# Optimization experiments

Hardware: AMD Instinct MI355X
Metric: run time of the kernel (lower is better)

Reference implementation:

```python
import jax, jax.numpy as jnp
import numpy as np

N = 20000   # nodes
E = 320000  # edges
F = 64      # input node features
H = 256     # hidden_layer_size
C = 10      # nbr_classes
G = 64      # graphs in the batch


def _lin(key, fan_in, fan_out):
    k1, k2 = jax.random.split(key)
    bound = 1.0 / np.sqrt(fan_in)
    W = jax.random.uniform(k1, (fan_in, fan_out), jnp.float32, -bound, bound)
    b = jax.random.uniform(k2, (fan_out,), jnp.float32, -bound, bound)
    return W, b


def setup_inputs() -> dict:
    key = jax.random.key(0)
    ks = jax.random.split(key, 10)
    x = jax.random.normal(ks[0], (N, F), jnp.float32)
    edge_index = jax.random.randint(ks[1], (2, E), 0, N)
    batch = jnp.sort(jax.random.randint(ks[2], (N,), 0, G))
    W1, b1 = _lin(ks[3], F, H)
    W2, b2 = _lin(ks[4], H, H)
    W3, b3 = _lin(ks[5], H, H)
    W4, b4 = _lin(ks[6], H, H)
    W5, b5 = _lin(ks[7], H, H)
    Wout, bout = _lin(ks[8], H, C)
    return {"x": x, "edge_index": edge_index, "batch": batch,
            "W1": W1, "b1": b1, "W2": W2, "b2": b2, "W3": W3, "b3": b3,
            "W4": W4, "b4": b4, "W5": W5, "b5": b5, "Wout": Wout, "bout": bout}


def reference(x, edge_index, batch, W1, b1, W2, b2, W3, b3, W4, b4, W5, b5, Wout, bout):
    # GCNConv (Kipf & Welling): add self-loops, D^{-1/2}(A+I)D^{-1/2} (X W) + b.
    # Dropout(p=0.5) is identity in eval mode (reference is deterministic).
    loop = jnp.arange(N)
    row = jnp.concatenate([edge_index[0], loop])  # source nodes, [E+N]
    col = jnp.concatenate([edge_index[1], loop])  # target nodes, [E+N]
    deg = jax.ops.segment_sum(jnp.ones(E + N, x.dtype), col, num_segments=N)
    dinv = jax.lax.rsqrt(deg)  # deg >= 1 thanks to self-loops
    norm = (dinv[row] * dinv[col])[:, None]  # [E+N, 1]

    def gcn_conv(h, W, b):
        m = (h @ W)[row] * norm                      # gather + normalize, [E+N, H]
        return jax.ops.segment_sum(m, col, num_segments=N) + b

    h = x
    for W, b in ((W1, b1), (W2, b2), (W3, b3), (W4, b4), (W5, b5)):
        h = jax.nn.relu(gcn_conv(h, W, b))

    # global_mean_pool over graph ids
    counts = jax.ops.segment_sum(jnp.ones(N, h.dtype), batch, num_segments=G)
    pooled = jax.ops.segment_sum(h, batch, num_segments=G) / jnp.maximum(counts, 1.0)[:, None]
    return pooled @ Wout + bout  # [G, C]
```

## Files before the change

### kernel.cpp

```cpp
#include <hip/hip_runtime.h>

#define NN 20000
#define NE 320000
#define FIN 64
#define HD 256
#define NC 10
#define NG 64
#define NB ((NN + 255) / 256)
#define EBMAX (NE + 15 * NN + 16)

typedef unsigned short u16;
typedef unsigned int u32;
typedef __attribute__((ext_vector_type(8))) short short8;
typedef __attribute__((ext_vector_type(4))) float f32x4;

__device__ __forceinline__ float bf2f(u16 u) {
    union { u32 i; float f; } v; v.i = ((u32)u) << 16; return v.f;
}
__device__ __forceinline__ u16 f2bf(float f) {
    union { float f; u32 i; } v; v.f = f;
    u32 r = v.i + 0x7fffu + ((v.i >> 16) & 1u);
    return (u16)(r >> 16);
}

__global__ void k_degpad(const int* __restrict__ col, int* __restrict__ degi,
                         const int* __restrict__ batch, int* __restrict__ gstart,
                         u32* __restrict__ ebuf32) {
    int i = blockIdx.x * 256 + threadIdx.x;
    if (i < NE) atomicAdd(&degi[col[i]], 1);
    if (i < NN) {
        int b = batch[i];
        int prev = (i == 0) ? -1 : batch[i - 1];
        if (b != prev) gstart[b] = i;
    }
    if (i < EBMAX / 2) ebuf32[i] = 0x4E204E20u;
}

__global__ __launch_bounds__(256) void k_scan1(const int* __restrict__ degi,
                                               int* __restrict__ rowptr,
                                               int* __restrict__ bsum) {
    int t = threadIdx.x;
    int i = blockIdx.x * 256 + t;
    int v = (i < NN) ? ((degi[i] + 15) & ~15) : 0;
    int lane = t & 63, wid = t >> 6;
    int x = v;
#pragma unroll
    for (int off = 1; off < 64; off <<= 1) {
        int y = __shfl_up(x, off);
        if (lane >= off) x += y;
    }
    __shared__ int ws[4];
    if (lane == 63) ws[wid] = x;
    __syncthreads();
    int woff = 0;
    for (int w = 0; w < wid; ++w) woff += ws[w];
    if (i < NN) rowptr[i] = woff + x - v;
    if (t == 255) bsum[blockIdx.x] = woff + x;
}

__global__ void k_scan3(const int* __restrict__ degi, const int* __restrict__ bsum,
                        int* __restrict__ rowptr, int* __restrict__ cursor,
                        float* __restrict__ dinv,
                        const float* __restrict__ x, u16* __restrict__ u0) {
    __shared__ int pref[NB];
    if (threadIdx.x < NB) pref[threadIdx.x] = bsum[threadIdx.x];
    __syncthreads();
    if (threadIdx.x == 0) {
        int run = 0;
        for (int k = 0; k < NB; ++k) { int t = pref[k]; pref[k] = run; run += t; }
    }
    __syncthreads();
    int i = blockIdx.x * 256 + threadIdx.x;
    if (i < NN) {
        int dg = degi[i];
        int rp = rowptr[i] + pref[i >> 8];
        rowptr[i] = rp;
        cursor[i] = rp;
        dinv[i] = rsqrtf((float)(1 + dg));
        if (i == NN - 1) rowptr[NN] = rp + ((dg + 15) & ~15);
    }
    if (i < NN * FIN / 4) {
        int node = i >> 4;
        float d = rsqrtf((float)(1 + degi[node]));
        float4 v = *(const float4*)&x[(size_t)i * 4];
        u32 lo = (u32)f2bf(v.x * d) | ((u32)f2bf(v.y * d) << 16);
        u32 hi = (u32)f2bf(v.z * d) | ((u32)f2bf(v.w * d) << 16);
        *(uint2*)&u0[(size_t)i * 4] = make_uint2(lo, hi);
    }
    if (blockIdx.x == 0 && threadIdx.x < FIN) u0[(size_t)NN * FIN + threadIdx.x] = 0;
}

__global__ void k_fill(const int* __restrict__ row, const int* __restrict__ col,
                       int* __restrict__ cursor, u16* __restrict__ ebuf) {
    int e = blockIdx.x * 256 + threadIdx.x;
    if (e < NE) {
        int c = col[e];
        int pos = atomicAdd(&cursor[c], 1);
        ebuf[pos] = (u16)row[e];
    }
}

__global__ __launch_bounds__(256) void k_trans(const float* __restrict__ W0, const float* __restrict__ W1,
                                               const float* __restrict__ W2, const float* __restrict__ W3,
                                               const float* __restrict__ W4,
                                               u16* __restrict__ T0, u16* __restrict__ T1,
                                               u16* __restrict__ T2, u16* __restrict__ T3,
                                               u16* __restrict__ T4) {
    int l = blockIdx.z;
    const float* W = (l == 0) ? W0 : (l == 1) ? W1 : (l == 2) ? W2 : (l == 3) ? W3 : W4;
    u16* T = (l == 0) ? T0 : (l == 1) ? T1 : (l == 2) ? T2 : (l == 3) ? T3 : T4;
    int K = (l == 0) ? FIN : HD;
    int k0 = blockIdx.x * 32;
    if (k0 >= K) return;
    int n0 = blockIdx.y * 32;
    __shared__ float tile[32][33];
    int tx = threadIdx.x & 31, ty = threadIdx.x >> 5;
#pragma unroll
    for (int r = 0; r < 32; r += 8)
        tile[ty + r][tx] = W[(size_t)(k0 + ty + r) * HD + n0 + tx];
    __syncthreads();
#pragma unroll
    for (int r = 0; r < 32; r += 8)
        T[(size_t)(n0 + ty + r) * K + k0 + tx] = f2bf(tile[tx][ty + r]);
}

__global__ __launch_bounds__(512, 8) void k_fused(const u16* __restrict__ U,
                                                  const int* __restrict__ rowptr,
                                                  const u16* __restrict__ ebuf,
                                                  const float* __restrict__ dinv,
                                                  const u16* __restrict__ Wt,
                                                  const float* __restrict__ bias,
                                                  u16* __restrict__ O,
                                                  int K, int scaleOut) {
    __shared__ u16 Asm[16][264];
    __shared__ float bs[HD];
    const int m0 = blockIdx.x * 16;
    const int t = threadIdx.x;
    const int wave = t >> 6;
    const int lane = t & 63;
    if (t < HD) bs[t] = bias[t];
    if (blockIdx.x == 0 && t < HD) O[(size_t)NN * HD + t] = 0;

    if (K == HD) {
        const int grp = lane >> 4;
        const int seg = lane & 15;
        for (int tk = 0; tk < 4; ++tk) {
            const int task = wave + tk * 8;
            const int row = task & 15;
            const int n = m0 + row;
            const int fbase = (task >> 4) * 128 + seg * 8;
            const int s = rowptr[n], e = rowptr[n + 1];
            float acc[8];
            if (grp == 0) {
                uint4 v = *(const uint4*)&U[(size_t)n * HD + fbase];
                acc[0] = bf2f((u16)(v.x & 0xffff)); acc[1] = bf2f((u16)(v.x >> 16));
                acc[2] = bf2f((u16)(v.y & 0xffff)); acc[3] = bf2f((u16)(v.y >> 16));
                acc[4] = bf2f((u16)(v.z & 0xffff)); acc[5] = bf2f((u16)(v.z >> 16));
                acc[6] = bf2f((u16)(v.w & 0xffff)); acc[7] = bf2f((u16)(v.w >> 16));
            } else {
#pragma unroll
                for (int k = 0; k < 8; ++k) acc[k] = 0.f;
            }
            for (int j = s; j < e; j += 16) {
                uint2 idv = *(const uint2*)&ebuf[j + grp * 4];
                int r0 = (int)(idv.x & 0xffff), r1 = (int)(idv.x >> 16);
                int r2 = (int)(idv.y & 0xffff), r3 = (int)(idv.y >> 16);
                uint4 v[4];
                v[0] = *(const uint4*)&U[(size_t)r0 * HD + fbase];
                v[1] = *(const uint4*)&U[(size_t)r1 * HD + fbase];
                v[2] = *(const uint4*)&U[(size_t)r2 * HD + fbase];
                v[3] = *(const uint4*)&U[(size_t)r3 * HD + fbase];
#pragma unroll
                for (int k = 0; k < 4; ++k) {
                    acc[0] += bf2f((u16)(v[k].x & 0xffff)); acc[1] += bf2f((u16)(v[k].x >> 16));
                    acc[2] += bf2f((u16)(v[k].y & 0xffff)); acc[3] += bf2f((u16)(v[k].y >> 16));
                    acc[4] += bf2f((u16)(v[k].z & 0xffff)); acc[5] += bf2f((u16)(v[k].z >> 16));
                    acc[6] += bf2f((u16)(v[k].w & 0xffff)); acc[7] += bf2f((u16)(v[k].w >> 16));
                }
            }
#pragma unroll
            for (int k = 0; k < 8; ++k) {
                acc[k] += __shfl_xor(acc[k], 16);
                acc[k] += __shfl_xor(acc[k], 32);
            }
            if (grp == 0) {
                float d = dinv[n];
                uint4 o;
                o.x = (u32)f2bf(acc[0] * d) | ((u32)f2bf(acc[1] * d) << 16);
                o.y = (u32)f2bf(acc[2] * d) | ((u32)f2bf(acc[3] * d) << 16);
                o.z = (u32)f2bf(acc[4] * d) | ((u32)f2bf(acc[5] * d) << 16);
                o.w = (u32)f2bf(acc[6] * d) | ((u32)f2bf(acc[7] * d) << 16);
                *(uint4*)&Asm[row][fbase] = o;
            }
        }
    } else {
        const int grp = lane >> 3;
        const int seg = lane & 7;
        for (int task = wave; task < 16; task += 8) {
            const int n = m0 + task;
            const int s = rowptr[n], e = rowptr[n + 1];
            float acc[8];
            if (grp == 0) {
                uint4 v = *(const uint4*)&U[(size_t)n * FIN + seg * 8];
                acc[0] = bf2f((u16)(v.x & 0xffff)); acc[1] = bf2f((u16)(v.x >> 16));
                acc[2] = bf2f((u16)(v.y & 0xffff)); acc[3] = bf2f((u16)(v.y >> 16));
                acc[4] = bf2f((u16)(v.z & 0xffff)); acc[5] = bf2f((u16)(v.z >> 16));
                acc[6] = bf2f((u16)(v.w & 0xffff)); acc[7] = bf2f((u16)(v.w >> 16));
            } else {
#pragma unroll
                for (int k = 0; k < 8; ++k) acc[k] = 0.f;
            }
            for (int j = s; j < e; j += 16) {
                int r0 = (int)ebuf[j + grp];
                int r1 = (int)ebuf[j + 8 + grp];
                uint4 v0 = *(const uint4*)&U[(size_t)r0 * FIN + seg * 8];
                uint4 v1 = *(const uint4*)&U[(size_t)r1 * FIN + seg * 8];
                acc[0] += bf2f((u16)(v0.x & 0xffff)); acc[1] += bf2f((u16)(v0.x >> 16));
                acc[2] += bf2f((u16)(v0.y & 0xffff)); acc[3] += bf2f((u16)(v0.y >> 16));
                acc[4] += bf2f((u16)(v0.z & 0xffff)); acc[5] += bf2f((u16)(v0.z >> 16));
                acc[6] += bf2f((u16)(v0.w & 0xffff)); acc[7] += bf2f((u16)(v0.w >> 16));
                acc[0] += bf2f((u16)(v1.x & 0xffff)); acc[1] += bf2f((u16)(v1.x >> 16));
                acc[2] += bf2f((u16)(v1.y & 0xffff)); acc[3] += bf2f((u16)(v1.y >> 16));
                acc[4] += bf2f((u16)(v1.z & 0xffff)); acc[5] += bf2f((u16)(v1.z >> 16));
                acc[6] += bf2f((u16)(v1.w & 0xffff)); acc[7] += bf2f((u16)(v1.w >> 16));
            }
#pragma unroll
            for (int off = 8; off < 64; off <<= 1)
#pragma unroll
                for (int k = 0; k < 8; ++k) acc[k] += __shfl_xor(acc[k], off);
            if (grp == 0) {
                float d = dinv[n];
                uint4 o;
                o.x = (u32)f2bf(acc[0] * d) | ((u32)f2bf(acc[1] * d) << 16);
                o.y = (u32)f2bf(acc[2] * d) | ((u32)f2bf(acc[3] * d) << 16);
                o.z = (u32)f2bf(acc[4] * d) | ((u32)f2bf(acc[5] * d) << 16);
                o.w = (u32)f2bf(acc[6] * d) | ((u32)f2bf(acc[7] * d) << 16);
                *(uint4*)&Asm[task][seg * 8] = o;
            }
        }
    }
    __syncthreads();

    const int quad = lane >> 4;
    const int l16 = lane & 15;
    const int n0 = wave * 32;
    f32x4 acc[2];
#pragma unroll
    for (int j = 0; j < 2; ++j) acc[j] = (f32x4){0.f, 0.f, 0.f, 0.f};

#pragma unroll 2
    for (int k0 = 0; k0 < K; k0 += 32) {
        short8 a = *(const short8*)&Asm[l16][k0 + quad * 8];
        short8 b0 = *(const short8*)&Wt[(size_t)(n0 + l16) * K + k0 + quad * 8];
        short8 b1 = *(const short8*)&Wt[(size_t)(n0 + 16 + l16) * K + k0 + quad * 8];
        acc[0] = __builtin_amdgcn_mfma_f32_16x16x32_bf16(a, b0, acc[0], 0, 0, 0);
        acc[1] = __builtin_amdgcn_mfma_f32_16x16x32_bf16(a, b1, acc[1], 0, 0, 0);
    }
#pragma unroll
    for (int r = 0; r < 4; ++r) {
        int m = m0 + quad * 4 + r;
        float d = scaleOut ? dinv[m] : 1.0f;
#pragma unroll
        for (int j = 0; j < 2; ++j) {
            int n = n0 + j * 16 + l16;
            float val = fmaxf(acc[j][r] + bs[n], 0.f) * d;
            O[(size_t)m * HD + n] = f2bf(val);
        }
    }
}

__global__ __launch_bounds__(512) void k_poolout(const u16* __restrict__ h,
                                                 const int* __restrict__ gstart,
                                                 const float* __restrict__ Wout,
                                                 const float* __restrict__ bout,
                                                 float* __restrict__ out) {
    int g = blockIdx.x;
    int t = threadIdx.x;
    int f = t & (HD - 1);
    int half = t >> 8;
    __shared__ float pp[2][HD];
    __shared__ float pooled[HD];
    __shared__ float part[NC][16];
    __shared__ int s_se[2];
    if (t == 0) {
        int st = gstart[g];
        int en = NN;
        for (int gg = g + 1; gg < NG; ++gg) en = min(en, gstart[gg]);
        s_se[0] = st; s_se[1] = en;
    }
    __syncthreads();
    int st = s_se[0], en = s_se[1];
    float a0 = 0.f, a1 = 0.f, a2 = 0.f, a3 = 0.f;
    int n = st + half;
    for (; n + 6 < en; n += 8) {
        a0 += bf2f(h[(size_t)n * HD + f]);
        a1 += bf2f(h[(size_t)(n + 2) * HD + f]);
        a2 += bf2f(h[(size_t)(n + 4) * HD + f]);
        a3 += bf2f(h[(size_t)(n + 6) * HD + f]);
    }
    for (; n < en; n += 2) a0 += bf2f(h[(size_t)n * HD + f]);
    pp[half][f] = a0 + a1 + a2 + a3;
    __syncthreads();
    if (t < HD) {
        float inv = 1.0f / (float)max(en - st, 1);
        pooled[t] = (pp[0][t] + pp[1][t]) * inv;
    }
    __syncthreads();
    if (t < NC * 16) {
        int c = t >> 4, l16 = t & 15;
        float s = 0.f;
        for (int ff = l16; ff < HD; ff += 16)
            s = fmaf(pooled[ff], Wout[(size_t)ff * NC + c], s);
        part[c][l16] = s;
    }
    __syncthreads();
    if (t < NC) {
        float s = 0.f;
#pragma unroll
        for (int k = 0; k < 16; ++k) s += part[t][k];
        out[(size_t)g * NC + t] = s + bout[t];
    }
}

extern "C" void kernel_launch(void* const* d_in, const int* in_sizes, int n_in,
                              void* d_out, int out_size, void* d_ws, size_t ws_size,
                              hipStream_t stream) {
    const float* x     = (const float*)d_in[0];
    const int*   ei    = (const int*)d_in[1];
    const int*   batch = (const int*)d_in[2];
    const float* Wl[5] = {(const float*)d_in[3], (const float*)d_in[5], (const float*)d_in[7],
                          (const float*)d_in[9], (const float*)d_in[11]};
    const float* bl[5] = {(const float*)d_in[4], (const float*)d_in[6], (const float*)d_in[8],
                          (const float*)d_in[10], (const float*)d_in[12]};
    const float* Wout = (const float*)d_in[13];
    const float* bout = (const float*)d_in[14];
    float* out = (float*)d_out;

    const int* row = ei;
    const int* col = ei + NE;

    char* p = (char*)d_ws;
    auto take = [&](size_t bytes) { char* q = p; p += (bytes + 255) & ~(size_t)255; return q; };
    float* dinv   = (float*)take(NN * 4);
    int*   degi   = (int*)take(NN * 4);
    int*   rowptr = (int*)take((NN + 1) * 4);
    int*   cursor = (int*)take(NN * 4);
    int*   bsum   = (int*)take(NB * 4);
    u16*   ebuf   = (u16*)take(EBMAX * 2);
    int*   gstart = (int*)take(NG * 4);
    u16*   Wt[5];
    for (int l = 0; l < 5; ++l) Wt[l] = (u16*)take((size_t)HD * HD * 2);
    u16*   B1     = (u16*)take((size_t)(NN + 1) * HD * 2);
    u16*   B2     = (u16*)take((size_t)(NN + 1) * HD * 2);

    hipMemsetAsync(degi, 0, NN * 4, stream);
    hipMemsetAsync(gstart, 0x7F, NG * 4, stream);
    k_degpad<<<(NE + 255) / 256, 256, 0, stream>>>(col, degi, batch, gstart, (u32*)ebuf);
    k_scan1<<<NB, 256, 0, stream>>>(degi, rowptr, bsum);
    k_scan3<<<(NN * FIN / 4 + 255) / 256, 256, 0, stream>>>(degi, bsum, rowptr, cursor, dinv, x, B1);
    k_fill<<<(NE + 255) / 256, 256, 0, stream>>>(row, col, cursor, ebuf);
    dim3 tGrid(8, 8, 5);
    k_trans<<<tGrid, 256, 0, stream>>>(Wl[0], Wl[1], Wl[2], Wl[3], Wl[4],
                                       Wt[0], Wt[1], Wt[2], Wt[3], Wt[4]);

    const int fGrid = NN / 16;
    k_fused<<<fGrid, 512, 0, stream>>>(B1, rowptr, ebuf, dinv, Wt[0], bl[0], B2, FIN, 1);
    k_fused<<<fGrid, 512, 0, stream>>>(B2, rowptr, ebuf, dinv, Wt[1], bl[1], B1, HD, 1);
    k_fused<<<fGrid, 512, 0, stream>>>(B1, rowptr, ebuf, dinv, Wt[2], bl[2], B2, HD, 1);
    k_fused<<<fGrid, 512, 0, stream>>>(B2, rowptr, ebuf, dinv, Wt[3], bl[3], B1, HD, 1);
    k_fused<<<fGrid, 512, 0, stream>>>(B1, rowptr, ebuf, dinv, Wt[4], bl[4], B2, HD, 0);

    k_poolout<<<NG, 512, 0, stream>>>(B2, gstart, Wout, bout, out);
}
```

Baseline: 367.6 us.

## Software-pipeline neighbor gathers across tasks and stage weights through LDS

The 256-wide aggregation now reads all row pointers and the first edge-index batch up front, then prefetches the next task's first neighbor rows and self row while the current task accumulates. Inside each task the next edge-index chunk is loaded before the current rows are summed. The MFMA loop now copies each 32-wide K slice of the transposed weights into a new shared buffer with two barriers per step, instead of each wave reading weights straight from global memory. Occupancy hint drops from 8 to 6 to fit the extra registers and LDS, which may reduce latency hiding, and the per-slice barriers add sync cost.

```diff
diff --git a/kernel.cpp b/kernel.cpp
--- a/kernel.cpp
+++ b/kernel.cpp
@@ -21,6 +21,21 @@
     union { float f; u32 i; } v; v.f = f;
     u32 r = v.i + 0x7fffu + ((v.i >> 16) & 1u);
     return (u16)(r >> 16);
+}
+
+__device__ __forceinline__ void accum8(float* acc, const uint4& v) {
+    acc[0] += bf2f((u16)(v.x & 0xffff)); acc[1] += bf2f((u16)(v.x >> 16));
+    acc[2] += bf2f((u16)(v.y & 0xffff)); acc[3] += bf2f((u16)(v.y >> 16));
+    acc[4] += bf2f((u16)(v.z & 0xffff)); acc[5] += bf2f((u16)(v.z >> 16));
+    acc[6] += bf2f((u16)(v.w & 0xffff)); acc[7] += bf2f((u16)(v.w >> 16));
+}
+__device__ __forceinline__ void loadrows(uint4* v, uint2 id, const u16* __restrict__ U, int fb) {
+    int r0 = (int)(id.x & 0xffff), r1 = (int)(id.x >> 16);
+    int r2 = (int)(id.y & 0xffff), r3 = (int)(id.y >> 16);
+    v[0] = *(const uint4*)&U[(size_t)r0 * HD + fb];
+    v[1] = *(const uint4*)&U[(size_t)r1 * HD + fb];
+    v[2] = *(const uint4*)&U[(size_t)r2 * HD + fb];
+    v[3] = *(const uint4*)&U[(size_t)r3 * HD + fb];
 }
 
 __global__ void k_degpad(const int* __restrict__ col, int* __restrict__ degi,
@@ -124,7 +139,7 @@
         T[(size_t)(n0 + ty + r) * K + k0 + tx] = f2bf(tile[tx][ty + r]);
 }
 
-__global__ __launch_bounds__(512, 8) void k_fused(const u16* __restrict__ U,
+__global__ __launch_bounds__(512, 6) void k_fused(const u16* __restrict__ U,
                                                   const int* __restrict__ rowptr,
                                                   const u16* __restrict__ ebuf,
                                                   const float* __restrict__ dinv,
@@ -133,6 +148,7 @@
                                                   u16* __restrict__ O,
                                                   int K, int scaleOut) {
     __shared__ u16 Asm[16][264];
+    __shared__ u16 Bsm[256][40];
     __shared__ float bs[HD];
     const int m0 = blockIdx.x * 16;
     const int t = threadIdx.x;
@@ -144,39 +160,58 @@
     if (K == HD) {
         const int grp = lane >> 4;
         const int seg = lane & 15;
+        int n_[4], s_[4], e_[4], fb_[4];
+#pragma unroll
         for (int tk = 0; tk < 4; ++tk) {
             const int task = wave + tk * 8;
-            const int row = task & 15;
-            const int n = m0 + row;
-            const int fbase = (task >> 4) * 128 + seg * 8;
-            const int s = rowptr[n], e = rowptr[n + 1];
+            n_[tk] = m0 + (task & 15);
+            fb_[tk] = (task >> 4) * 128 + seg * 8;
+        }
+#pragma unroll
+        for (int tk = 0; tk < 4; ++tk) {
+            s_[tk] = rowptr[n_[tk]];
+            e_[tk] = rowptr[n_[tk] + 1];
+        }
+        uint2 id_[4];
+#pragma unroll
+        for (int tk = 0; tk < 4; ++tk)
+            id_[tk] = (s_[tk] < e_[tk]) ? *(const uint2*)&ebuf[s_[tk] + grp * 4]
+                                        : make_uint2(0x4E204E20u, 0x4E204E20u);
+        uint4 va[4], sla;
+        loadrows(va, id_[0], U, fb_[0]);
+        sla = *(const uint4*)&U[(size_t)n_[0] * HD + fb_[0]];
+#pragma unroll
+        for (int tk = 0; tk < 4; ++tk) {
+            uint4 vb[4], slb;
+            if (tk < 3) {
+                loadrows(vb, id_[tk + 1], U, fb_[tk + 1]);
+                slb = *(const uint4*)&U[(size_t)n_[tk + 1] * HD + fb_[tk + 1]];
+            } else {
+                vb[0] = vb[1] = vb[2] = vb[3] = make_uint4(0u, 0u, 0u, 0u);
+                slb = make_uint4(0u, 0u, 0u, 0u);
+            }
             float acc[8];
             if (grp == 0) {
-                uint4 v = *(const uint4*)&U[(size_t)n * HD + fbase];
-                acc[0] = bf2f((u16)(v.x & 0xffff)); acc[1] = bf2f((u16)(v.x >> 16));
-                acc[2] = bf2f((u16)(v.y & 0xffff)); acc[3] = bf2f((u16)(v.y >> 16));
-                acc[4] = bf2f((u16)(v.z & 0xffff)); acc[5] = bf2f((u16)(v.z >> 16));
-                acc[6] = bf2f((u16)(v.w & 0xffff)); acc[7] = bf2f((u16)(v.w >> 16));
+                acc[0] = bf2f((u16)(sla.x & 0xffff)); acc[1] = bf2f((u16)(sla.x >> 16));
+                acc[2] = bf2f((u16)(sla.y & 0xffff)); acc[3] = bf2f((u16)(sla.y >> 16));
+                acc[4] = bf2f((u16)(sla.z & 0xffff)); acc[5] = bf2f((u16)(sla.z >> 16));
+                acc[6] = bf2f((u16)(sla.w & 0xffff)); acc[7] = bf2f((u16)(sla.w >> 16));
             } else {
 #pragma unroll
                 for (int k = 0; k < 8; ++k) acc[k] = 0.f;
             }
-            for (int j = s; j < e; j += 16) {
-                uint2 idv = *(const uint2*)&ebuf[j + grp * 4];
-                int r0 = (int)(idv.x & 0xffff), r1 = (int)(idv.x >> 16);
-                int r2 = (int)(idv.y & 0xffff), r3 = (int)(idv.y >> 16);
-                uint4 v[4];
-                v[0] = *(const uint4*)&U[(size_t)r0 * HD + fbase];
-                v[1] = *(const uint4*)&U[(size_t)r1 * HD + fbase];
-                v[2] = *(const uint4*)&U[(size_t)r2 * HD + fbase];
-                v[3] = *(const uint4*)&U[(size_t)r3 * HD + fbase];
-#pragma unroll
-                for (int k = 0; k < 4; ++k) {
-                    acc[0] += bf2f((u16)(v[k].x & 0xffff)); acc[1] += bf2f((u16)(v[k].x >> 16));
-                    acc[2] += bf2f((u16)(v[k].y & 0xffff)); acc[3] += bf2f((u16)(v[k].y >> 16));
-                    acc[4] += bf2f((u16)(v[k].z & 0xffff)); acc[5] += bf2f((u16)(v[k].z >> 16));
-                    acc[6] += bf2f((u16)(v[k].w & 0xffff)); acc[7] += bf2f((u16)(v[k].w >> 16));
-                }
+            int j = s_[tk] + 16;
+            bool more = j < e_[tk];
+            uint2 idn = make_uint2(0x4E204E20u, 0x4E204E20u);
+            if (more) idn = *(const uint2*)&ebuf[j + grp * 4];
+            accum8(acc, va[0]); accum8(acc, va[1]); accum8(acc, va[2]); accum8(acc, va[3]);
+            while (more) {
+                uint4 vx[4];
+                loadrows(vx, idn, U, fb_[tk]);
+                j += 16;
+                more = j < e_[tk];
+                if (more) idn = *(const uint2*)&ebuf[j + grp * 4];
+                accum8(acc, vx[0]); accum8(acc, vx[1]); accum8(acc, vx[2]); accum8(acc, vx[3]);
             }
 #pragma unroll
             for (int k = 0; k < 8; ++k) {
@@ -184,14 +219,17 @@
                 acc[k] += __shfl_xor(acc[k], 32);
             }
             if (grp == 0) {
-                float d = dinv[n];
+                float d = dinv[n_[tk]];
                 uint4 o;
                 o.x = (u32)f2bf(acc[0] * d) | ((u32)f2bf(acc[1] * d) << 16);
                 o.y = (u32)f2bf(acc[2] * d) | ((u32)f2bf(acc[3] * d) << 16);
                 o.z = (u32)f2bf(acc[4] * d) | ((u32)f2bf(acc[5] * d) << 16);
                 o.w = (u32)f2bf(acc[6] * d) | ((u32)f2bf(acc[7] * d) << 16);
-                *(uint4*)&Asm[row][fbase] = o;
-            }
+                *(uint4*)&Asm[n_[tk] - m0][fb_[tk]] = o;
+            }
+#pragma unroll
+            for (int k = 0; k < 4; ++k) va[k] = vb[k];
+            sla = slb;
         }
     } else {
         const int grp = lane >> 3;
@@ -215,14 +253,8 @@
                 int r1 = (int)ebuf[j + 8 + grp];
                 uint4 v0 = *(const uint4*)&U[(size_t)r0 * FIN + seg * 8];
                 uint4 v1 = *(const uint4*)&U[(size_t)r1 * FIN + seg * 8];
-                acc[0] += bf2f((u16)(v0.x & 0xffff)); acc[1] += bf2f((u16)(v0.x >> 16));
-                acc[2] += bf2f((u16)(v0.y & 0xffff)); acc[3] += bf2f((u16)(v0.y >> 16));
-                acc[4] += bf2f((u16)(v0.z & 0xffff)); acc[5] += bf2f((u16)(v0.z >> 16));
-                acc[6] += bf2f((u16)(v0.w & 0xffff)); acc[7] += bf2f((u16)(v0.w >> 16));
-                acc[0] += bf2f((u16)(v1.x & 0xffff)); acc[1] += bf2f((u16)(v1.x >> 16));
-                acc[2] += bf2f((u16)(v1.y & 0xffff)); acc[3] += bf2f((u16)(v1.y >> 16));
-                acc[4] += bf2f((u16)(v1.z & 0xffff)); acc[5] += bf2f((u16)(v1.z >> 16));
-                acc[6] += bf2f((u16)(v1.w & 0xffff)); acc[7] += bf2f((u16)(v1.w >> 16));
+                accum8(acc, v0);
+                accum8(acc, v1);
             }
 #pragma unroll
             for (int off = 8; off < 64; off <<= 1)
@@ -248,13 +280,24 @@
 #pragma unroll
     for (int j = 0; j < 2; ++j) acc[j] = (f32x4){0.f, 0.f, 0.f, 0.f};
 
-#pragma unroll 2
     for (int k0 = 0; k0 < K; k0 += 32) {
+        {
+            int r = t >> 1, h16 = (t & 1) * 16;
+#pragma unroll
+            for (int j = 0; j < 2; ++j) {
+                float4 v = *(const float4*)&Wt[(size_t)r * K + k0 + h16 + j * 8];
+                *(float4*)&Bsm[r][h16 + j * 8] = v;
+            }
+        }
+        __syncthreads();
         short8 a = *(const short8*)&Asm[l16][k0 + quad * 8];
-        short8 b0 = *(const short8*)&Wt[(size_t)(n0 + l16) * K + k0 + quad * 8];
-        short8 b1 = *(const short8*)&Wt[(size_t)(n0 + 16 + l16) * K + k0 + quad * 8];
-        acc[0] = __builtin_amdgcn_mfma_f32_16x16x32_bf16(a, b0, acc[0], 0, 0, 0);
-        acc[1] = __builtin_amdgcn_mfma_f32_16x16x32_bf16(a, b1, acc[1], 0, 0, 0);
+        short8 b[2];
+#pragma unroll
+        for (int j = 0; j < 2; ++j) b[j] = *(const short8*)&Bsm[n0 + j * 16 + l16][quad * 8];
+#pragma unroll
+        for (int j = 0; j < 2; ++j)
+            acc[j] = __builtin_amdgcn_mfma_f32_16x16x32_bf16(a, b[j], acc[j], 0, 0, 0);
+        __syncthreads();
     }
 #pragma unroll
     for (int r = 0; r < 4; ++r) {
```

Result: slower. 414.5 us (+12.8%).

## Pad edge lists to 8, shuffle-broadcast neighbor ids, stage weights in LDS

Applied to the files above, without the earlier changes.

Each node's edge list is now padded to a multiple of 8 instead of 16. This cuts the wasted gathers of the zero sentinel row in both aggregation paths. In the 256-wide path, the first 8 lanes load neighbor ids once and broadcast them with shuffles, and the row/half task mapping is reordered. The MFMA loop now stages each 32-wide K-slice of the transposed weights through a new shared-memory buffer with barriers, instead of each wave reading its slice straight from global memory. The extra LDS and barriers may lower occupancy and add sync overhead, since there is little reuse of that slice across waves.

```diff
diff --git a/kernel.cpp b/kernel.cpp
--- a/kernel.cpp
+++ b/kernel.cpp
@@ -7,7 +7,7 @@
 #define NC 10
 #define NG 64
 #define NB ((NN + 255) / 256)
-#define EBMAX (NE + 15 * NN + 16)
+#define EBMAX (NE + 7 * NN + 8)
 
 typedef unsigned short u16;
 typedef unsigned int u32;
@@ -21,6 +21,12 @@
     union { float f; u32 i; } v; v.f = f;
     u32 r = v.i + 0x7fffu + ((v.i >> 16) & 1u);
     return (u16)(r >> 16);
+}
+__device__ __forceinline__ void accum8(float* acc, const uint4& v) {
+    acc[0] += bf2f((u16)(v.x & 0xffff)); acc[1] += bf2f((u16)(v.x >> 16));
+    acc[2] += bf2f((u16)(v.y & 0xffff)); acc[3] += bf2f((u16)(v.y >> 16));
+    acc[4] += bf2f((u16)(v.z & 0xffff)); acc[5] += bf2f((u16)(v.z >> 16));
+    acc[6] += bf2f((u16)(v.w & 0xffff)); acc[7] += bf2f((u16)(v.w >> 16));
 }
 
 __global__ void k_degpad(const int* __restrict__ col, int* __restrict__ degi,
@@ -41,7 +47,7 @@
                                                int* __restrict__ bsum) {
     int t = threadIdx.x;
     int i = blockIdx.x * 256 + t;
-    int v = (i < NN) ? ((degi[i] + 15) & ~15) : 0;
+    int v = (i < NN) ? ((degi[i] + 7) & ~7) : 0;
     int lane = t & 63, wid = t >> 6;
     int x = v;
 #pragma unroll
@@ -77,7 +83,7 @@
         rowptr[i] = rp;
         cursor[i] = rp;
         dinv[i] = rsqrtf((float)(1 + dg));
-        if (i == NN - 1) rowptr[NN] = rp + ((dg + 15) & ~15);
+        if (i == NN - 1) rowptr[NN] = rp + ((dg + 7) & ~7);
     }
     if (i < NN * FIN / 4) {
         int node = i >> 4;
@@ -133,6 +139,7 @@
                                                   u16* __restrict__ O,
                                                   int K, int scaleOut) {
     __shared__ u16 Asm[16][264];
+    __shared__ u16 Bsm[256][40];
     __shared__ float bs[HD];
     const int m0 = blockIdx.x * 16;
     const int t = threadIdx.x;
@@ -144,11 +151,10 @@
     if (K == HD) {
         const int grp = lane >> 4;
         const int seg = lane & 15;
-        for (int tk = 0; tk < 4; ++tk) {
-            const int task = wave + tk * 8;
-            const int row = task & 15;
+        for (int task = wave; task < 32; task += 8) {
+            const int row = task >> 1;
             const int n = m0 + row;
-            const int fbase = (task >> 4) * 128 + seg * 8;
+            const int fbase = (task & 1) * 128 + seg * 8;
             const int s = rowptr[n], e = rowptr[n + 1];
             float acc[8];
             if (grp == 0) {
@@ -161,22 +167,16 @@
 #pragma unroll
                 for (int k = 0; k < 8; ++k) acc[k] = 0.f;
             }
-            for (int j = s; j < e; j += 16) {
-                uint2 idv = *(const uint2*)&ebuf[j + grp * 4];
-                int r0 = (int)(idv.x & 0xffff), r1 = (int)(idv.x >> 16);
-                int r2 = (int)(idv.y & 0xffff), r3 = (int)(idv.y >> 16);
-                uint4 v[4];
-                v[0] = *(const uint4*)&U[(size_t)r0 * HD + fbase];
-                v[1] = *(const uint4*)&U[(size_t)r1 * HD + fbase];
-                v[2] = *(const uint4*)&U[(size_t)r2 * HD + fbase];
-                v[3] = *(const uint4*)&U[(size_t)r3 * HD + fbase];
-#pragma unroll
-                for (int k = 0; k < 4; ++k) {
-                    acc[0] += bf2f((u16)(v[k].x & 0xffff)); acc[1] += bf2f((u16)(v[k].x >> 16));
-                    acc[2] += bf2f((u16)(v[k].y & 0xffff)); acc[3] += bf2f((u16)(v[k].y >> 16));
-                    acc[4] += bf2f((u16)(v[k].z & 0xffff)); acc[5] += bf2f((u16)(v[k].z >> 16));
-                    acc[6] += bf2f((u16)(v[k].w & 0xffff)); acc[7] += bf2f((u16)(v[k].w >> 16));
+            for (int j = s; j < e; j += 8) {
+                int myid = (lane < 8) ? (int)ebuf[j + lane] : 0;
+                uint4 v[2];
+#pragma unroll
+                for (int k = 0; k < 2; ++k) {
+                    int r = __shfl(myid, grp * 2 + k);
+                    v[k] = *(const uint4*)&U[(size_t)r * HD + fbase];
                 }
+                accum8(acc, v[0]);
+                accum8(acc, v[1]);
             }
 #pragma unroll
             for (int k = 0; k < 8; ++k) {
@@ -210,19 +210,10 @@
 #pragma unroll
                 for (int k = 0; k < 8; ++k) acc[k] = 0.f;
             }
-            for (int j = s; j < e; j += 16) {
+            for (int j = s; j < e; j += 8) {
                 int r0 = (int)ebuf[j + grp];
-                int r1 = (int)ebuf[j + 8 + grp];
                 uint4 v0 = *(const uint4*)&U[(size_t)r0 * FIN + seg * 8];
-                uint4 v1 = *(const uint4*)&U[(size_t)r1 * FIN + seg * 8];
-                acc[0] += bf2f((u16)(v0.x & 0xffff)); acc[1] += bf2f((u16)(v0.x >> 16));
-                acc[2] += bf2f((u16)(v0.y & 0xffff)); acc[3] += bf2f((u16)(v0.y >> 16));
-                acc[4] += bf2f((u16)(v0.z & 0xffff)); acc[5] += bf2f((u16)(v0.z >> 16));
-                acc[6] += bf2f((u16)(v0.w & 0xffff)); acc[7] += bf2f((u16)(v0.w >> 16));
-                acc[0] += bf2f((u16)(v1.x & 0xffff)); acc[1] += bf2f((u16)(v1.x >> 16));
-                acc[2] += bf2f((u16)(v1.y & 0xffff)); acc[3] += bf2f((u16)(v1.y >> 16));
-                acc[4] += bf2f((u16)(v1.z & 0xffff)); acc[5] += bf2f((u16)(v1.z >> 16));
-                acc[6] += bf2f((u16)(v1.w & 0xffff)); acc[7] += bf2f((u16)(v1.w >> 16));
+                accum8(acc, v0);
             }
 #pragma unroll
             for (int off = 8; off < 64; off <<= 1)
@@ -248,13 +239,24 @@
 #pragma unroll
     for (int j = 0; j < 2; ++j) acc[j] = (f32x4){0.f, 0.f, 0.f, 0.f};
 
-#pragma unroll 2
     for (int k0 = 0; k0 < K; k0 += 32) {
+        {
+            int r = t >> 1, h16 = (t & 1) * 16;
+#pragma unroll
+            for (int j = 0; j < 2; ++j) {
+                float4 v = *(const float4*)&Wt[(size_t)r * K + k0 + h16 + j * 8];
+                *(float4*)&Bsm[r][h16 + j * 8] = v;
+            }
+        }
+        __syncthreads();
         short8 a = *(const short8*)&Asm[l16][k0 + quad * 8];
-        short8 b0 = *(const short8*)&Wt[(size_t)(n0 + l16) * K + k0 + quad * 8];
-        short8 b1 = *(const short8*)&Wt[(size_t)(n0 + 16 + l16) * K + k0 + quad * 8];
-        acc[0] = __builtin_amdgcn_mfma_f32_16x16x32_bf16(a, b0, acc[0], 0, 0, 0);
-        acc[1] = __builtin_amdgcn_mfma_f32_16x16x32_bf16(a, b1, acc[1], 0, 0, 0);
+        short8 b[2];
+#pragma unroll
+        for (int j = 0; j < 2; ++j) b[j] = *(const short8*)&Bsm[n0 + j * 16 + l16][quad * 8];
+#pragma unroll
+        for (int j = 0; j < 2; ++j)
+            acc[j] = __builtin_amdgcn_mfma_f32_16x16x32_bf16(a, b[j], acc[j], 0, 0, 0);
+        __syncthreads();
     }
 #pragma unroll
     for (int r = 0; r < 4; ++r) {
```

Measured after the change: 339.3 us. -7.7%, faster.
